# Performance work log

Hardware: AMD Instinct MI355X
Metric: run time of the kernel (lower is better)

## Reference

```python
import jax, jax.numpy as jnp
import numpy as np

SIGMAS = (0.02, 0.01, 0.008)   # self.sig
SIGMA_N = 0.5                  # self.sig_n
COORD_SCALE = 0.05             # keep distances commensurate with sigmas


def setup_inputs() -> dict:
    key = jax.random.key(0)
    k1, k2, k3 = jax.random.split(key, 3)
    B, Vn, Fn = 2, 5000, 6144
    predictions = jax.random.uniform(k1, (B, Vn, 3), dtype=jnp.float32) * COORD_SCALE
    targets = jax.random.uniform(k2, (B, Vn, 3), dtype=jnp.float32) * COORD_SCALE
    faces = jax.random.randint(k3, (Fn, 3), 0, Vn, dtype=jnp.int32)
    return {"predictions": predictions, "targets": targets, "faces": faces}


def _mesh_quantities(V, F):
    # face centers C [F,3], areas L [F,1], unit normals Nn [F,3]
    v0, v1, v2 = V[F[:, 0]], V[F[:, 1]], V[F[:, 2]]
    C = (v0 + v1 + v2) / 3.0
    N = 0.5 * jnp.cross(v1 - v0, v2 - v0)
    L = jnp.sqrt((N * N).sum(-1, keepdims=True) + 1e-24)
    return C, L, N / L


def _varifold_prod(C1, L1, N1, C2, L2, N2, sigma, sigma_n):
    # <mu1, mu2> = sum_ij L1_i L2_j exp(-|c_i-c_j|^2/sigma^2) exp((<n_i,n_j>-1)/sigma_n^2)
    d2 = ((C1[:, None, :] - C2[None, :, :]) ** 2).sum(-1)          # [F,F]
    ndot = N1 @ N2.T                                               # [F,F]
    K = jnp.exp(-d2 / (sigma * sigma) + (ndot - 1.0) / (sigma_n * sigma_n))
    return (L1[:, 0] * (K @ L2[:, 0])).sum()


def reference(predictions, targets, faces):
    def per_sample(Vs, Vt):
        Cs, Ls, Ns = _mesh_quantities(Vs, faces)
        Ct, Lt, Nt = _mesh_quantities(Vt, faces)
        li = jnp.float32(0.0)
        for sig in SIGMAS:  # small fixed set of sigmas
            w = (sig / SIGMAS[0]) ** 2
            pss = _varifold_prod(Cs, Ls, Ns, Cs, Ls, Ns, sig, SIGMA_N)
            pst = _varifold_prod(Cs, Ls, Ns, Ct, Lt, Nt, sig, SIGMA_N)
            ptt = _varifold_prod(Ct, Lt, Nt, Ct, Lt, Nt, sig, SIGMA_N)
            li = li + w * (pss - 2.0 * pst + ptt)
        return li

    L = jax.vmap(per_sample)(predictions, targets)  # [B]
    return jnp.mean(L)
```

## Files before the change

### kernel.cpp

```cpp
#include <hip/hip_runtime.h>

#define F_FACES 6144
#define VN      5000

#define SC_F    30.02806022f
#define SN_F    2.40224481f
#define C4_F    5.7707801635558535f

__device__ __forceinline__ float fast_exp2(float x) {
    float r;
    asm("v_exp_f32 %0, %1" : "=v"(r) : "v"(x));
    return r;
}

#define CELLS_OFF_FLOATS (4 * F_FACES * 2 * 4)

__global__ __launch_bounds__(256) void mesh_prep(
    const float* __restrict__ pred, const float* __restrict__ targ,
    const int* __restrict__ faces, float4* __restrict__ ws4,
    float* __restrict__ cells)
{
    const int f = blockIdx.x * 256 + threadIdx.x;
    const int m = blockIdx.y;
    if (blockIdx.x == 0 && m == 0 && threadIdx.x < 64)
        cells[threadIdx.x * 16] = 0.0f;
    if (f >= F_FACES) return;

    const int b = m >> 1, which = m & 1;
    const float* V = (which ? targ : pred) + b * (VN * 3);

    const int i0 = faces[3 * f + 0];
    const int i1 = faces[3 * f + 1];
    const int i2 = faces[3 * f + 2];

    const float v0x = V[3 * i0 + 0], v0y = V[3 * i0 + 1], v0z = V[3 * i0 + 2];
    const float v1x = V[3 * i1 + 0], v1y = V[3 * i1 + 1], v1z = V[3 * i1 + 2];
    const float v2x = V[3 * i2 + 0], v2y = V[3 * i2 + 1], v2z = V[3 * i2 + 2];

    const float Cx = (v0x + v1x + v2x) * (1.0f / 3.0f);
    const float Cy = (v0y + v1y + v2y) * (1.0f / 3.0f);
    const float Cz = (v0z + v1z + v2z) * (1.0f / 3.0f);

    const float e1x = v1x - v0x, e1y = v1y - v0y, e1z = v1z - v0z;
    const float e2x = v2x - v0x, e2y = v2y - v0y, e2z = v2z - v0z;

    const float Nx = 0.5f * (e1y * e2z - e1z * e2y);
    const float Ny = 0.5f * (e1z * e2x - e1x * e2z);
    const float Nz = 0.5f * (e1x * e2y - e1y * e2x);

    const float l2  = Nx * Nx + Ny * Ny + Nz * Nz + 1e-24f;
    const float L   = sqrtf(l2);
    const float inv = 1.0f / L;

    const float Csx = Cx * SC_F, Csy = Cy * SC_F, Csz = Cz * SC_F;
    const float a   = -(Csx * Csx + Csy * Csy + Csz * Csz);
    const float s   = inv * SN_F;

    const long base = (long)(m * F_FACES + f) * 2;
    ws4[base + 0] = make_float4(Csx, Csy, Csz, a);
    ws4[base + 1] = make_float4(Nx * s, Ny * s, Nz * s, log2f(L) - C4_F);
}

#define BLK       128
#define IT        4
#define I_ROWS    (BLK * IT)
#define I_TILES   (F_FACES / I_ROWS)
#define W_TRI_Q   39936
#define TRI_TOTAL (4 * W_TRI_Q)
#define TOTAL_COLS 307200
#define N_BLOCKS  12288
#define CPB       25

__global__ __launch_bounds__(BLK, 8) void varifold_pairs(
    const float4* __restrict__ ws4, float* __restrict__ cells)
{
    __shared__ float4 sAB[2 * CPB];
    __shared__ float  red[2];

    const int tid = threadIdx.x;
    int col = blockIdx.x * CPB;
    int remaining = CPB;
    float total = 0.0f;

    int cur_key = -1;
    float C2x[IT], C2y[IT], C2z[IT], Ai[IT];
    float Nix[IT], Niy[IT], Niz[IT], Li[IT];
    float acc[IT];

    while (remaining > 0) {
        int c, b, it, j, r, bandLeft;
        if (col < TRI_TOTAL) {
            const int q = col / W_TRI_Q;
            r = col - q * W_TRI_Q;
            c = (q >> 1) ? 2 : 0; b = q & 1;
            it = 0;
            int w = F_FACES;
            while (r >= w) { r -= w; ++it; w -= I_ROWS; }
            j = it * I_ROWS + r;
            bandLeft = w - r;
        } else {
            const int lin = col - TRI_TOTAL;
            const int band = lin / F_FACES;
            r = lin - band * F_FACES;
            j = r;
            b = band / I_TILES; it = band - (band / I_TILES) * I_TILES;
            c = 1;
            bandLeft = F_FACES - r;
        }
        const bool strad = (c != 1) && (r < I_ROWS);
        int segLen = min(remaining, bandLeft);
        if (strad) segLen = min(segLen, I_ROWS - r);
        const float wOut = (c == 1) ? -1.0f : (strad ? 0.5f : 1.0f);
        const int m1 = 2 * b + (c == 2 ? 1 : 0);
        const int m2 = 2 * b + (c >= 1 ? 1 : 0);
        const float4* P1 = ws4 + (long)m1 * (F_FACES * 2);
        const float4* P2 = ws4 + (long)m2 * (F_FACES * 2);
        const int iBase = it * I_ROWS;

        const int key = m1 * 16 + it;
        if (key != cur_key) {
            cur_key = key;
#pragma unroll
            for (int k = 0; k < IT; ++k) {
                const int i = iBase + k * BLK + tid;
                const float4 A  = P1[2 * i + 0];
                const float4 Bv = P1[2 * i + 1];
                C2x[k] = 2.0f * A.x; C2y[k] = 2.0f * A.y; C2z[k] = 2.0f * A.z;
                Ai[k]  = A.w;
                Nix[k] = Bv.x; Niy[k] = Bv.y; Niz[k] = Bv.z;
                Li[k]  = fast_exp2(Bv.w + C4_F);
            }
        }
#pragma unroll
        for (int k = 0; k < IT; ++k) acc[k] = 0.0f;

        __syncthreads();
        if (tid < 2 * segLen) sAB[tid] = P2[2 * j + tid];
        __syncthreads();

        if (!strad) {
            for (int jj = 0; jj < segLen; ++jj) {
                const float4 a4 = sAB[2 * jj + 0];
                const float4 b4 = sAB[2 * jj + 1];
#pragma unroll
                for (int k = 0; k < IT; ++k) {
                    float rr = fmaf(C2x[k], a4.x, a4.w);
                    rr = fmaf(C2y[k], a4.y, rr);
                    rr = fmaf(C2z[k], a4.z, rr);
                    const float t0 = fast_exp2(rr + Ai[k]);
                    float n = fmaf(Nix[k], b4.x, b4.w);
                    n = fmaf(Niy[k], b4.y, n);
                    n = fmaf(Niz[k], b4.z, n);
                    const float en = fast_exp2(n);
                    const float t2  = t0 * t0;
                    const float t4  = t2 * t2;
                    const float t8  = t4 * t4;
                    const float t16 = t8 * t8;
                    const float t24 = t16 * t8;
                    const float t25 = t24 * t0;
                    float p = fmaf(0.25f, t16, t4);
                    p = fmaf(0.16f, t25, p);
                    acc[k] = fmaf(en, p, acc[k]);
                }
            }
        } else {
            for (int jj = 0; jj < segLen; ++jj) {
                const float4 a4 = sAB[2 * jj + 0];
                const float4 b4 = sAB[2 * jj + 1];
                const int jg = j + jj;
#pragma unroll
                for (int k = 0; k < IT; ++k) {
                    const int i = iBase + k * BLK + tid;
                    float rr = fmaf(C2x[k], a4.x, a4.w);
                    rr = fmaf(C2y[k], a4.y, rr);
                    rr = fmaf(C2z[k], a4.z, rr);
                    const float t0 = fast_exp2(rr + Ai[k]);
                    float n = fmaf(Nix[k], b4.x, b4.w);
                    n = fmaf(Niy[k], b4.y, n);
                    n = fmaf(Niz[k], b4.z, n);
                    const float en = fast_exp2(n);
                    const float t2  = t0 * t0;
                    const float t4  = t2 * t2;
                    const float t8  = t4 * t4;
                    const float t16 = t8 * t8;
                    const float t24 = t16 * t8;
                    const float t25 = t24 * t0;
                    float p = fmaf(0.25f, t16, t4);
                    p = fmaf(0.16f, t25, p);
                    float fw = (jg > i) ? 2.0f : 0.0f;
                    fw = (jg == i) ? 1.0f : fw;
                    acc[k] = fmaf(fw * en, p, acc[k]);
                }
            }
        }

        float part = 0.0f;
#pragma unroll
        for (int k = 0; k < IT; ++k) part = fmaf(acc[k], Li[k], part);
        total = fmaf(wOut, part, total);

        col += segLen; remaining -= segLen;
    }

#pragma unroll
    for (int off = 32; off; off >>= 1) total += __shfl_xor(total, off);
    if ((tid & 63) == 0) red[tid >> 6] = total;
    __syncthreads();
    if (tid == 0)
        atomicAdd(&cells[(blockIdx.x & 63) * 16], red[0] + red[1]);
}

__global__ __launch_bounds__(64) void finalize_sum(
    const float* __restrict__ cells, float* __restrict__ out)
{
    float v = cells[threadIdx.x * 16];
#pragma unroll
    for (int off = 32; off; off >>= 1) v += __shfl_xor(v, off);
    if (threadIdx.x == 0) out[0] = v;
}

extern "C" void kernel_launch(void* const* d_in, const int* in_sizes, int n_in,
                              void* d_out, int out_size, void* d_ws, size_t ws_size,
                              hipStream_t stream) {
    const float* pred  = (const float*)d_in[0];
    const float* targ  = (const float*)d_in[1];
    const int*   faces = (const int*)d_in[2];
    float*       out   = (float*)d_out;
    float4*      ws4   = (float4*)d_ws;
    float*       cells = (float*)d_ws + CELLS_OFF_FLOATS;

    dim3 g1(F_FACES / 256, 4);
    mesh_prep<<<g1, 256, 0, stream>>>(pred, targ, faces, ws4, cells);

    varifold_pairs<<<dim3(N_BLOCKS), dim3(BLK), 0, stream>>>(ws4, cells);

    finalize_sum<<<dim3(1), dim3(64), 0, stream>>>(cells, out);
}
```

Measured before the change: 130.2 us.

## Fuse mesh preprocessing into pair kernel and replace atomics with per-block partials

Removes the separate mesh_prep kernel, so each pair block recomputes face centres, normals and areas directly from the vertex and face arrays, for both its resident row tile and its column segment. Atomics into 64 cells are replaced by one partial per block, which the finalize kernel reduces with 256 threads. sqrt and divide become v_rsq, and log2 becomes v_log. This saves a launch and the workspace round-trip, at the cost of redundant gather-heavy recomputation in every block and a lower launch-bounds occupancy hint.

```diff
diff --git a/kernel.cpp b/kernel.cpp
--- a/kernel.cpp
+++ b/kernel.cpp
@@ -8,27 +8,20 @@
 #define C4_F    5.7707801635558535f
 
 __device__ __forceinline__ float fast_exp2(float x) {
-    float r;
-    asm("v_exp_f32 %0, %1" : "=v"(r) : "v"(x));
-    return r;
-}
-
-#define CELLS_OFF_FLOATS (4 * F_FACES * 2 * 4)
-
-__global__ __launch_bounds__(256) void mesh_prep(
-    const float* __restrict__ pred, const float* __restrict__ targ,
-    const int* __restrict__ faces, float4* __restrict__ ws4,
-    float* __restrict__ cells)
+    float r; asm("v_exp_f32 %0, %1" : "=v"(r) : "v"(x)); return r;
+}
+__device__ __forceinline__ float fast_rsq(float x) {
+    float r; asm("v_rsq_f32 %0, %1" : "=v"(r) : "v"(x)); return r;
+}
+__device__ __forceinline__ float fast_log2(float x) {
+    float r; asm("v_log_f32 %0, %1" : "=v"(r) : "v"(x)); return r;
+}
+
+__device__ __forceinline__ void face_quant(
+    const float* __restrict__ V, const int* __restrict__ faces, int f,
+    float& Csx, float& Csy, float& Csz, float& a,
+    float& Nsx, float& Nsy, float& Nsz, float& L)
 {
-    const int f = blockIdx.x * 256 + threadIdx.x;
-    const int m = blockIdx.y;
-    if (blockIdx.x == 0 && m == 0 && threadIdx.x < 64)
-        cells[threadIdx.x * 16] = 0.0f;
-    if (f >= F_FACES) return;
-
-    const int b = m >> 1, which = m & 1;
-    const float* V = (which ? targ : pred) + b * (VN * 3);
-
     const int i0 = faces[3 * f + 0];
     const int i1 = faces[3 * f + 1];
     const int i2 = faces[3 * f + 2];
@@ -49,16 +42,13 @@
     const float Nz = 0.5f * (e1x * e2y - e1y * e2x);
 
     const float l2  = Nx * Nx + Ny * Ny + Nz * Nz + 1e-24f;
-    const float L   = sqrtf(l2);
-    const float inv = 1.0f / L;
-
-    const float Csx = Cx * SC_F, Csy = Cy * SC_F, Csz = Cz * SC_F;
-    const float a   = -(Csx * Csx + Csy * Csy + Csz * Csz);
-    const float s   = inv * SN_F;
-
-    const long base = (long)(m * F_FACES + f) * 2;
-    ws4[base + 0] = make_float4(Csx, Csy, Csz, a);
-    ws4[base + 1] = make_float4(Nx * s, Ny * s, Nz * s, log2f(L) - C4_F);
+    const float irt = fast_rsq(l2);
+    L = l2 * irt;
+    const float s = irt * SN_F;
+
+    Csx = Cx * SC_F; Csy = Cy * SC_F; Csz = Cz * SC_F;
+    a   = -(Csx * Csx + Csy * Csy + Csz * Csz);
+    Nsx = Nx * s; Nsy = Ny * s; Nsz = Nz * s;
 }
 
 #define BLK       128
@@ -67,12 +57,12 @@
 #define I_TILES   (F_FACES / I_ROWS)
 #define W_TRI_Q   39936
 #define TRI_TOTAL (4 * W_TRI_Q)
-#define TOTAL_COLS 307200
 #define N_BLOCKS  12288
 #define CPB       25
 
-__global__ __launch_bounds__(BLK, 8) void varifold_pairs(
-    const float4* __restrict__ ws4, float* __restrict__ cells)
+__global__ __launch_bounds__(BLK, 6) void varifold_pairs(
+    const float* __restrict__ pred, const float* __restrict__ targ,
+    const int* __restrict__ faces, float* __restrict__ parts)
 {
     __shared__ float4 sAB[2 * CPB];
     __shared__ float  red[2];
@@ -113,8 +103,8 @@
         const float wOut = (c == 1) ? -1.0f : (strad ? 0.5f : 1.0f);
         const int m1 = 2 * b + (c == 2 ? 1 : 0);
         const int m2 = 2 * b + (c >= 1 ? 1 : 0);
-        const float4* P1 = ws4 + (long)m1 * (F_FACES * 2);
-        const float4* P2 = ws4 + (long)m2 * (F_FACES * 2);
+        const float* V1 = ((m1 & 1) ? targ : pred) + (m1 >> 1) * (VN * 3);
+        const float* V2 = ((m2 & 1) ? targ : pred) + (m2 >> 1) * (VN * 3);
         const int iBase = it * I_ROWS;
 
         const int key = m1 * 16 + it;
@@ -122,20 +112,23 @@
             cur_key = key;
 #pragma unroll
             for (int k = 0; k < IT; ++k) {
-                const int i = iBase + k * BLK + tid;
-                const float4 A  = P1[2 * i + 0];
-                const float4 Bv = P1[2 * i + 1];
-                C2x[k] = 2.0f * A.x; C2y[k] = 2.0f * A.y; C2z[k] = 2.0f * A.z;
-                Ai[k]  = A.w;
-                Nix[k] = Bv.x; Niy[k] = Bv.y; Niz[k] = Bv.z;
-                Li[k]  = fast_exp2(Bv.w + C4_F);
+                float cx, cy, cz, a, nx, ny, nz, L;
+                face_quant(V1, faces, iBase + k * BLK + tid,
+                           cx, cy, cz, a, nx, ny, nz, L);
+                C2x[k] = 2.0f * cx; C2y[k] = 2.0f * cy; C2z[k] = 2.0f * cz;
+                Ai[k] = a; Nix[k] = nx; Niy[k] = ny; Niz[k] = nz; Li[k] = L;
             }
         }
 #pragma unroll
         for (int k = 0; k < IT; ++k) acc[k] = 0.0f;
 
         __syncthreads();
-        if (tid < 2 * segLen) sAB[tid] = P2[2 * j + tid];
+        if (tid < segLen) {
+            float cx, cy, cz, a, nx, ny, nz, L;
+            face_quant(V2, faces, j + tid, cx, cy, cz, a, nx, ny, nz, L);
+            sAB[2 * tid + 0] = make_float4(cx, cy, cz, a);
+            sAB[2 * tid + 1] = make_float4(nx, ny, nz, fast_log2(L) - C4_F);
+        }
         __syncthreads();
 
         if (!strad) {
@@ -206,17 +199,20 @@
     for (int off = 32; off; off >>= 1) total += __shfl_xor(total, off);
     if ((tid & 63) == 0) red[tid >> 6] = total;
     __syncthreads();
-    if (tid == 0)
-        atomicAdd(&cells[(blockIdx.x & 63) * 16], red[0] + red[1]);
-}
-
-__global__ __launch_bounds__(64) void finalize_sum(
-    const float* __restrict__ cells, float* __restrict__ out)
+    if (tid == 0) parts[blockIdx.x] = red[0] + red[1];
+}
+
+__global__ __launch_bounds__(256) void finalize_sum(
+    const float* __restrict__ parts, float* __restrict__ out)
 {
-    float v = cells[threadIdx.x * 16];
+    __shared__ float s[4];
+    float v = 0.0f;
+    for (int i = threadIdx.x; i < N_BLOCKS; i += 256) v += parts[i];
 #pragma unroll
     for (int off = 32; off; off >>= 1) v += __shfl_xor(v, off);
-    if (threadIdx.x == 0) out[0] = v;
+    if ((threadIdx.x & 63) == 0) s[threadIdx.x >> 6] = v;
+    __syncthreads();
+    if (threadIdx.x == 0) out[0] = s[0] + s[1] + s[2] + s[3];
 }
 
 extern "C" void kernel_launch(void* const* d_in, const int* in_sizes, int n_in,
@@ -226,13 +222,8 @@
     const float* targ  = (const float*)d_in[1];
     const int*   faces = (const int*)d_in[2];
     float*       out   = (float*)d_out;
-    float4*      ws4   = (float4*)d_ws;
-    float*       cells = (float*)d_ws + CELLS_OFF_FLOATS;
-
-    dim3 g1(F_FACES / 256, 4);
-    mesh_prep<<<g1, 256, 0, stream>>>(pred, targ, faces, ws4, cells);
-
-    varifold_pairs<<<dim3(N_BLOCKS), dim3(BLK), 0, stream>>>(ws4, cells);
-
-    finalize_sum<<<dim3(1), dim3(64), 0, stream>>>(cells, out);
-}
+    float*       parts = (float*)d_ws;
+
+    varifold_pairs<<<dim3(N_BLOCKS), dim3(BLK), 0, stream>>>(pred, targ, faces, parts);
+    finalize_sum<<<dim3(1), dim3(256), 0, stream>>>(parts, out);
+}
```

Result: slower. 152.6 us (+17.2%).
